# Kernel tuning notes

Measured on AMD Instinct MI355X. Metric: run time of the kernel, lower is better.

Reference implementation:

```python
import jax, jax.numpy as jnp
import numpy as np

EPS = 1e-5

def _weight_quant(w):
    # BitNet b1.58: per-tensor ternary quantization with STE.
    scale = 1.0 / jnp.maximum(jnp.mean(jnp.abs(w)), EPS)
    wq = jnp.clip(jnp.round(w * scale), -1.0, 1.0) / scale
    return w + jax.lax.stop_gradient(wq - w)

def _act_quant(x):
    # per-token int8 absmax quantization with STE.
    scale = 127.0 / jnp.maximum(jnp.max(jnp.abs(x), axis=-1, keepdims=True), EPS)
    xq = jnp.clip(jnp.round(x * scale), -128.0, 127.0) / scale
    return x + jax.lax.stop_gradient(xq - x)

def _bitlinear(x, w):
    # x: [..., in], w: [out, in] (torch layout)
    return jnp.einsum('bsd,hd->bsh', _act_quant(x), _weight_quant(w))

def setup_inputs() -> dict:
    key = jax.random.key(0)
    k1, k2, k3, k4 = jax.random.split(key, 4)
    B, S, D, H = 4, 2048, 2048, 5632
    x = jax.random.normal(k1, (B, S, D), dtype=jnp.float32)
    w1 = jax.random.normal(k2, (H, D), dtype=jnp.float32) * 0.02
    w2 = jax.random.normal(k3, (H, D), dtype=jnp.float32) * 0.02
    w3 = jax.random.normal(k4, (D, H), dtype=jnp.float32) * 0.02
    return {"x": x, "w1": w1, "w2": w2, "w3": w3}

def reference(x, w1, w2, w3):
    gate = jax.nn.silu(_bitlinear(x, w1))   # [B,S,H]
    up = _bitlinear(x, w2)                  # [B,S,H]
    h = gate * up                           # [B,S,H]
    return _bitlinear(h, w3)                # [B,S,D]
```

## Files before the change

### kernel.cpp

```cpp
#include <hip/hip_runtime.h>
#include <hip/hip_bf16.h>
#include <math.h>

#define EPSQ 1e-5f

typedef __attribute__((ext_vector_type(4))) int i32x4;

__device__ __forceinline__ void gload_lds16(const void* g, void* l) {
  __builtin_amdgcn_global_load_lds(
      (__attribute__((address_space(1))) void*)g,
      (__attribute__((address_space(3))) void*)l, 16, 0, 0);
}

__device__ __forceinline__ int clampi8(float v, float lo, float hi) {
  return (int)rintf(fminf(hi, fmaxf(lo, v)));
}

__global__ void wabs3_kernel(const float* __restrict__ w1, const float* __restrict__ w2,
                             const float* __restrict__ w3, int n4,
                             double* __restrict__ sums) {
  const float* w = (blockIdx.y == 0) ? w1 : (blockIdx.y == 1) ? w2 : w3;
  __shared__ double sm[256];
  const float4* w4 = (const float4*)w;
  double acc = 0.0;
  const int stride = gridDim.x * blockDim.x;
  for (int i = blockIdx.x * blockDim.x + threadIdx.x; i < n4; i += stride) {
    float4 v = w4[i];
    acc += (double)fabsf(v.x) + (double)fabsf(v.y) + (double)fabsf(v.z) + (double)fabsf(v.w);
  }
  sm[threadIdx.x] = acc;
  __syncthreads();
  for (int s = 128; s > 0; s >>= 1) {
    if ((int)threadIdx.x < s) sm[threadIdx.x] += sm[threadIdx.x + s];
    __syncthreads();
  }
  if (threadIdx.x == 0) atomicAdd(sums + blockIdx.y, sm[0]);
}

__global__ void wquant3_kernel(const float* __restrict__ w1, const float* __restrict__ w2,
                               const float* __restrict__ w3, int n4,
                               const double* __restrict__ sums, double inv_n,
                               unsigned int* __restrict__ q1, unsigned int* __restrict__ q2,
                               unsigned int* __restrict__ q3) {
  const int wsel = blockIdx.y;
  const float* w = (wsel == 0) ? w1 : (wsel == 1) ? w2 : w3;
  unsigned int* wq = (wsel == 0) ? q1 : (wsel == 1) ? q2 : q3;
  const float s = (float)fmax(sums[wsel] * inv_n, (double)EPSQ);
  const float scale = 1.0f / s;
  const int i = blockIdx.x * blockDim.x + threadIdx.x;
  if (i >= n4) return;
  float4 v = ((const float4*)w)[i];
  const int b0 = clampi8(rintf(v.x * scale), -1.f, 1.f);
  const int b1 = clampi8(rintf(v.y * scale), -1.f, 1.f);
  const int b2 = clampi8(rintf(v.z * scale), -1.f, 1.f);
  const int b3 = clampi8(rintf(v.w * scale), -1.f, 1.f);
  wq[i] = (unsigned int)((b0 & 0xff) | ((b1 & 0xff) << 8) |
                         ((b2 & 0xff) << 16) | ((b3 & 0xff) << 24));
}

__global__ void aquant_kernel(const float* __restrict__ x, int K,
                              unsigned char* __restrict__ q, float* __restrict__ arow) {
  const int row = blockIdx.x;
  const int n4 = K >> 2;
  const float4* xr = (const float4*)(x + (size_t)row * K);
  float m = 0.f;
  for (int c = threadIdx.x; c < n4; c += blockDim.x) {
    float4 v = xr[c];
    m = fmaxf(m, fmaxf(fmaxf(fabsf(v.x), fabsf(v.y)), fmaxf(fabsf(v.z), fabsf(v.w))));
  }
  __shared__ float sm[256];
  sm[threadIdx.x] = m;
  __syncthreads();
  for (int s = 128; s > 0; s >>= 1) {
    if ((int)threadIdx.x < s) sm[threadIdx.x] = fmaxf(sm[threadIdx.x], sm[threadIdx.x + s]);
    __syncthreads();
  }
  const float mv = fmaxf(sm[0], EPSQ);
  const float scale = 127.0f / mv;
  if (threadIdx.x == 0) arow[row] = mv * (1.0f / 127.0f);
  unsigned int* qr = (unsigned int*)(q + (size_t)row * K);
  for (int c = threadIdx.x; c < n4; c += blockDim.x) {
    float4 v = xr[c];
    const int b0 = clampi8(v.x * scale, -128.f, 127.f);
    const int b1 = clampi8(v.y * scale, -128.f, 127.f);
    const int b2 = clampi8(v.z * scale, -128.f, 127.f);
    const int b3 = clampi8(v.w * scale, -128.f, 127.f);
    qr[c] = (unsigned int)((b0 & 0xff) | ((b1 & 0xff) << 8) |
                           ((b2 & 0xff) << 16) | ((b3 & 0xff) << 24));
  }
}

__global__ void aquant_pre_kernel(const float* __restrict__ x, int K,
                                  unsigned char* __restrict__ q, float* __restrict__ arow) {
  const int row = blockIdx.x;
  const float raw = arow[row];
  __syncthreads();
  const float mv = fmaxf(raw, EPSQ);
  const float scale = 127.0f / mv;
  if (threadIdx.x == 0) arow[row] = mv * (1.0f / 127.0f);
  const int n4 = K >> 2;
  const float4* xr = (const float4*)(x + (size_t)row * K);
  unsigned int* qr = (unsigned int*)(q + (size_t)row * K);
  for (int c = threadIdx.x; c < n4; c += blockDim.x) {
    float4 v = xr[c];
    const int b0 = clampi8(v.x * scale, -128.f, 127.f);
    const int b1 = clampi8(v.y * scale, -128.f, 127.f);
    const int b2 = clampi8(v.z * scale, -128.f, 127.f);
    const int b3 = clampi8(v.w * scale, -128.f, 127.f);
    qr[c] = (unsigned int)((b0 & 0xff) | ((b1 & 0xff) << 8) |
                           ((b2 & 0xff) << 16) | ((b3 & 0xff) << 24));
  }
}

#define BKP 64

#define PIPE_BARRIER(N)                                         \
  asm volatile("s_waitcnt vmcnt(" #N ")" ::: "memory");         \
  __builtin_amdgcn_s_barrier();                                 \
  asm volatile("" ::: "memory");

#define GU_SLOT 32768

__launch_bounds__(512, 2)
__global__ void gemm_gateup(const unsigned char* __restrict__ Aq,
                            const unsigned char* __restrict__ W1q,
                            const unsigned char* __restrict__ W2q,
                            const float* __restrict__ arow,
                            const double* __restrict__ wsum,
                            float* __restrict__ Hbuf,
                            float* __restrict__ hmax,
                            const int N, const int K,
                            const int MBb, const int NBb) {
  __shared__ char lds[3 * GU_SLOT];

  const int tid = threadIdx.x;
  const int lane = tid & 63;
  const int wid = tid >> 6;
  const int wm = wid >> 1;
  const int wn = wid & 1;

  const int total = MBb * NBb;
  int swz = blockIdx.x;
  if ((total & 7) == 0) swz = (swz & 7) * (total >> 3) + (swz >> 3);
  const int nb = swz % NBb;
  const int mb = swz / NBb;
  const int m0 = mb * 256;
  const int n0 = nb * 128;

  const unsigned char* Ab  = Aq  + (size_t)m0 * K;
  const unsigned char* B1b = W1q + (size_t)n0 * K;
  const unsigned char* B2b = W2q + (size_t)n0 * K;

  auto stage = [&](int kt, int s) {
    const int k0 = kt * BKP;
    char* base = lds + s * GU_SLOT;
#pragma unroll
    for (int is = 0; is < 2; ++is) {
      const int p = is * 8192 + wid * 1024 + lane * 16;
      const int r = p >> 6;
      const int c = ((p >> 4) & 3) ^ ((r >> 1) & 3);
      gload_lds16(Ab + (size_t)r * K + k0 + c * 16, base + is * 8192 + wid * 1024);
    }
    {
      const int p = wid * 1024 + lane * 16;
      const int r = p >> 6;
      const int c = ((p >> 4) & 3) ^ ((r >> 1) & 3);
      const size_t go = (size_t)r * K + k0 + c * 16;
      gload_lds16(B1b + go, base + 16384 + wid * 1024);
      gload_lds16(B2b + go, base + 24576 + wid * 1024);
    }
  };

  const int c16 = lane >> 4;
  int offA[4], offB1[4], offB2[4];
#pragma unroll
  for (int i = 0; i < 4; ++i) {
    const int row = wm * 64 + i * 16 + (lane & 15);
    offA[i] = row * 64 + ((c16 ^ ((row >> 1) & 3)) << 4);
  }
#pragma unroll
  for (int j = 0; j < 4; ++j) {
    const int n = wn * 64 + j * 16 + (lane & 15);
    const int o = n * 64 + ((c16 ^ ((n >> 1) & 3)) << 4);
    offB1[j] = 16384 + o;
    offB2[j] = 24576 + o;
  }

  i32x4 acc1[4][4] = {};
  i32x4 acc2[4][4] = {};

  const int NT = K / BKP;
  stage(0, 0);
  stage(1, 1);
  PIPE_BARRIER(4)

  int s = 0, s2 = 2;
  for (int t = 0; t < NT; ++t) {
    if (t + 2 < NT) stage(t + 2, s2);
    const char* sb = lds + s * GU_SLOT;
    i32x4 af[4], b1f[4], b2f[4];
#pragma unroll
    for (int i = 0; i < 4; ++i) af[i] = *(const i32x4*)(sb + offA[i]);
#pragma unroll
    for (int j = 0; j < 4; ++j) {
      b1f[j] = *(const i32x4*)(sb + offB1[j]);
      b2f[j] = *(const i32x4*)(sb + offB2[j]);
    }
    __builtin_amdgcn_s_setprio(1);
#pragma unroll
    for (int j = 0; j < 4; ++j)
#pragma unroll
      for (int i = 0; i < 4; ++i) {
        acc1[i][j] = __builtin_amdgcn_mfma_i32_16x16x64_i8(af[i], b1f[j], acc1[i][j], 0, 0, 0);
        acc2[i][j] = __builtin_amdgcn_mfma_i32_16x16x64_i8(af[i], b2f[j], acc2[i][j], 0, 0, 0);
      }
    __builtin_amdgcn_s_setprio(0);
    if (t + 2 < NT) {
      PIPE_BARRIER(4)
    } else if (t + 1 < NT) {
      PIPE_BARRIER(0)
    }
    s = (s == 2) ? 0 : s + 1;
    s2 = (s2 == 2) ? 0 : s2 + 1;
  }

  const double inv_n = 1.0 / 11534336.0;
  const float sw1 = (float)fmax(wsum[0] * inv_n, (double)EPSQ);
  const float sw2 = (float)fmax(wsum[1] * inv_n, (double)EPSQ);
#pragma unroll
  for (int i = 0; i < 4; ++i) {
    const int rb = m0 + wm * 64 + i * 16 + (lane >> 4) * 4;
#pragma unroll
    for (int qe = 0; qe < 4; ++qe) {
      const int grow = rb + qe;
      const float a = arow[grow];
      const float f1 = a * sw1;
      const float f2 = a * sw2;
      float* hr = Hbuf + (size_t)grow * N + n0 + wn * 64 + (lane & 15);
      float lmax = 0.f;
#pragma unroll
      for (int j = 0; j < 4; ++j) {
        const float y1 = (float)acc1[i][j][qe] * f1;
        const float y2 = (float)acc2[i][j][qe] * f2;
        const float h = (y1 / (1.0f + expf(-y1))) * y2;
        hr[j * 16] = h;
        lmax = fmaxf(lmax, fabsf(h));
      }
#pragma unroll
      for (int mk = 8; mk >= 1; mk >>= 1)
        lmax = fmaxf(lmax, __shfl_xor(lmax, mk, 64));
      if ((lane & 15) == 0)
        atomicMax((unsigned int*)(hmax + grow), __float_as_uint(lmax));
    }
  }
}

#define DN_SLOT 24576

__launch_bounds__(512, 2)
__global__ void gemm_down(const unsigned char* __restrict__ Aq,
                          const unsigned char* __restrict__ Wq,
                          const float* __restrict__ arow,
                          const double* __restrict__ wsum,
                          float* __restrict__ Out,
                          const int N, const int K,
                          const int MBb, const int NBb) {
  __shared__ char lds[3 * DN_SLOT];

  const int tid = threadIdx.x;
  const int lane = tid & 63;
  const int wid = tid >> 6;
  const int wm = wid >> 1;
  const int wn = wid & 1;

  const int total = MBb * NBb;
  int swz = blockIdx.x;
  if ((total & 7) == 0) swz = (swz & 7) * (total >> 3) + (swz >> 3);
  const int nb = swz % NBb;
  const int mb = swz / NBb;
  const int m0 = mb * 256;
  const int n0 = nb * 128;

  const unsigned char* Ab = Aq + (size_t)m0 * K;
  const unsigned char* Bb = Wq + (size_t)n0 * K;

  auto stage = [&](int kt, int s) {
    const int k0 = kt * BKP;
    char* base = lds + s * DN_SLOT;
#pragma unroll
    for (int is = 0; is < 2; ++is) {
      const int p = is * 8192 + wid * 1024 + lane * 16;
      const int r = p >> 6;
      const int c = ((p >> 4) & 3) ^ ((r >> 1) & 3);
      gload_lds16(Ab + (size_t)r * K + k0 + c * 16, base + is * 8192 + wid * 1024);
    }
    {
      const int p = wid * 1024 + lane * 16;
      const int r = p >> 6;
      const int c = ((p >> 4) & 3) ^ ((r >> 1) & 3);
      gload_lds16(Bb + (size_t)r * K + k0 + c * 16, base + 16384 + wid * 1024);
    }
  };

  const int c16 = lane >> 4;
  int offA[4], offB[4];
#pragma unroll
  for (int i = 0; i < 4; ++i) {
    const int row = wm * 64 + i * 16 + (lane & 15);
    offA[i] = row * 64 + ((c16 ^ ((row >> 1) & 3)) << 4);
  }
#pragma unroll
  for (int j = 0; j < 4; ++j) {
    const int n = wn * 64 + j * 16 + (lane & 15);
    offB[j] = 16384 + n * 64 + ((c16 ^ ((n >> 1) & 3)) << 4);
  }

  i32x4 acc[4][4] = {};

  const int NT = K / BKP;
  stage(0, 0);
  stage(1, 1);
  PIPE_BARRIER(3)

  int s = 0, s2 = 2;
  for (int t = 0; t < NT; ++t) {
    if (t + 2 < NT) stage(t + 2, s2);
    const char* sb = lds + s * DN_SLOT;
    i32x4 af[4], bf[4];
#pragma unroll
    for (int i = 0; i < 4; ++i) af[i] = *(const i32x4*)(sb + offA[i]);
#pragma unroll
    for (int j = 0; j < 4; ++j) bf[j] = *(const i32x4*)(sb + offB[j]);
    __builtin_amdgcn_s_setprio(1);
#pragma unroll
    for (int j = 0; j < 4; ++j)
#pragma unroll
      for (int i = 0; i < 4; ++i)
        acc[i][j] = __builtin_amdgcn_mfma_i32_16x16x64_i8(af[i], bf[j], acc[i][j], 0, 0, 0);
    __builtin_amdgcn_s_setprio(0);
    if (t + 2 < NT) {
      PIPE_BARRIER(3)
    } else if (t + 1 < NT) {
      PIPE_BARRIER(0)
    }
    s = (s == 2) ? 0 : s + 1;
    s2 = (s2 == 2) ? 0 : s2 + 1;
  }

  const double inv_n = 1.0 / 11534336.0;
  const float sw3 = (float)fmax(wsum[2] * inv_n, (double)EPSQ);
#pragma unroll
  for (int i = 0; i < 4; ++i) {
    const int rb = m0 + wm * 64 + i * 16 + (lane >> 4) * 4;
#pragma unroll
    for (int qe = 0; qe < 4; ++qe) {
      const int grow = rb + qe;
      const float f = arow[grow] * sw3;
      float* orow = Out + (size_t)grow * N + n0 + wn * 64 + (lane & 15);
#pragma unroll
      for (int j = 0; j < 4; ++j) {
        orow[j * 16] = (float)acc[i][j][qe] * f;
      }
    }
  }
}

extern "C" void kernel_launch(void* const* d_in, const int* in_sizes, int n_in,
                              void* d_out, int out_size, void* d_ws, size_t ws_size,
                              hipStream_t stream) {
  (void)n_in; (void)out_size;
  const float* x  = (const float*)d_in[0];
  const float* w1 = (const float*)d_in[1];
  const float* w2 = (const float*)d_in[2];
  const float* w3 = (const float*)d_in[3];
  float* out = (float*)d_out;

  const int D = 2048, H = 5632;
  const int M = in_sizes[0] / D;
  const long long NW = (long long)H * D;

  auto al = [](size_t v) { return (v + 255) & ~(size_t)255; };

  size_t off = 0;
  const size_t o_wsum = off; off += al(3 * sizeof(double));
  const size_t o_w1q  = off; off += al((size_t)NW);
  const size_t o_w2q  = off; off += al((size_t)NW);
  const size_t o_w3q  = off; off += al((size_t)NW);
  const size_t fixed = off;

  int Mc = 256;
  for (int cand = M; cand >= 256; cand >>= 1) {
    size_t need = fixed
                + al((size_t)cand * 4)
                + al((size_t)cand * 4)
                + al((size_t)cand * D)
                + al((size_t)cand * H * 4)
                + al((size_t)cand * H);
    if (need <= ws_size) { Mc = cand; break; }
  }

  size_t coff = fixed;
  const size_t o_arow1 = coff; coff += al((size_t)Mc * 4);
  const size_t o_arow2 = coff; coff += al((size_t)Mc * 4);
  const size_t o_qx    = coff; coff += al((size_t)Mc * D);
  const size_t o_hbuf  = coff; coff += al((size_t)Mc * H * 4);
  const size_t o_qh    = coff; coff += al((size_t)Mc * H);

  char* ws = (char*)d_ws;
  double* wsum        = (double*)(ws + o_wsum);
  unsigned char* w1q  = (unsigned char*)(ws + o_w1q);
  unsigned char* w2q  = (unsigned char*)(ws + o_w2q);
  unsigned char* w3q  = (unsigned char*)(ws + o_w3q);
  float* arow1        = (float*)(ws + o_arow1);
  float* arow2        = (float*)(ws + o_arow2);
  unsigned char* qx   = (unsigned char*)(ws + o_qx);
  float* hbuf         = (float*)(ws + o_hbuf);
  unsigned char* qh   = (unsigned char*)(ws + o_qh);

  hipMemsetAsync(wsum, 0, 3 * sizeof(double), stream);

  const int n4w = (int)(NW / 4);
  wabs3_kernel<<<dim3(1024, 3), 256, 0, stream>>>(w1, w2, w3, n4w, wsum);

  const double inv_n = 1.0 / (double)NW;
  wquant3_kernel<<<dim3(n4w / 256, 3), 256, 0, stream>>>(
      w1, w2, w3, n4w, wsum, inv_n,
      (unsigned int*)w1q, (unsigned int*)w2q, (unsigned int*)w3q);

  const int NBgu = H / 128;
  const int NBdn = D / 128;
  for (int c = 0; c < M; c += Mc) {
    const int MBb = Mc / 256;
    aquant_kernel<<<Mc, 256, 0, stream>>>(x + (size_t)c * D, D, qx, arow1);
    hipMemsetAsync(arow2, 0, (size_t)Mc * 4, stream);
    gemm_gateup<<<MBb * NBgu, 512, 0, stream>>>(qx, w1q, w2q, arow1, wsum,
                                                hbuf, arow2, H, D, MBb, NBgu);
    aquant_pre_kernel<<<Mc, 256, 0, stream>>>(hbuf, H, qh, arow2);
    gemm_down<<<MBb * NBdn, 512, 0, stream>>>(qh, w3q, arow2, wsum,
                                              out + (size_t)c * D, D, H, MBb, NBdn);
  }
}
```

Baseline: 492.8 us.

## Halve GEMM M-tile to 128 and replace atomic row-max with partial-max buffer

Both int8 GEMMs shrink their block tile from 256x128 to 128x128, with 8 waves arranged 2x4 and each wave computing a 64x32 subtile. This cuts LDS per block and doubles the grid, presumably to improve occupancy or load balance. The per-row absmax of the hidden activation is now written as per-slice partials into a new buffer and reduced inside the activation quantization kernel. That replaces the global atomicMax and the memset before it. In exchange, each block gets less operand reuse per loaded byte and the quantization kernel does an extra reduction pass.

```diff
diff --git a/kernel.cpp b/kernel.cpp
--- a/kernel.cpp
+++ b/kernel.cpp
@@ -91,11 +91,20 @@
 }
 
 __global__ void aquant_pre_kernel(const float* __restrict__ x, int K,
+                                  const float* __restrict__ hpart, int nslice,
                                   unsigned char* __restrict__ q, float* __restrict__ arow) {
   const int row = blockIdx.x;
-  const float raw = arow[row];
+  __shared__ float sm[256];
+  float m = 0.f;
+  for (int t = threadIdx.x; t < nslice; t += blockDim.x)
+    m = fmaxf(m, hpart[(size_t)row * nslice + t]);
+  sm[threadIdx.x] = m;
   __syncthreads();
-  const float mv = fmaxf(raw, EPSQ);
+  for (int s = 128; s > 0; s >>= 1) {
+    if ((int)threadIdx.x < s) sm[threadIdx.x] = fmaxf(sm[threadIdx.x], sm[threadIdx.x + s]);
+    __syncthreads();
+  }
+  const float mv = fmaxf(sm[0], EPSQ);
   const float scale = 127.0f / mv;
   if (threadIdx.x == 0) arow[row] = mv * (1.0f / 127.0f);
   const int n4 = K >> 2;
@@ -119,7 +128,7 @@
   __builtin_amdgcn_s_barrier();                                 \
   asm volatile("" ::: "memory");
 
-#define GU_SLOT 32768
+#define GU_SLOT 24576
 
 __launch_bounds__(512, 2)
 __global__ void gemm_gateup(const unsigned char* __restrict__ Aq,
@@ -128,7 +137,7 @@
                             const float* __restrict__ arow,
                             const double* __restrict__ wsum,
                             float* __restrict__ Hbuf,
-                            float* __restrict__ hmax,
+                            float* __restrict__ hpart,
                             const int N, const int K,
                             const int MBb, const int NBb) {
   __shared__ char lds[3 * GU_SLOT];
@@ -136,15 +145,15 @@
   const int tid = threadIdx.x;
   const int lane = tid & 63;
   const int wid = tid >> 6;
-  const int wm = wid >> 1;
-  const int wn = wid & 1;
+  const int wm = wid >> 2;
+  const int wn = wid & 3;
 
   const int total = MBb * NBb;
   int swz = blockIdx.x;
   if ((total & 7) == 0) swz = (swz & 7) * (total >> 3) + (swz >> 3);
   const int nb = swz % NBb;
   const int mb = swz / NBb;
-  const int m0 = mb * 256;
+  const int m0 = mb * 128;
   const int n0 = nb * 128;
 
   const unsigned char* Ab  = Aq  + (size_t)m0 * K;
@@ -154,61 +163,53 @@
   auto stage = [&](int kt, int s) {
     const int k0 = kt * BKP;
     char* base = lds + s * GU_SLOT;
-#pragma unroll
-    for (int is = 0; is < 2; ++is) {
-      const int p = is * 8192 + wid * 1024 + lane * 16;
-      const int r = p >> 6;
-      const int c = ((p >> 4) & 3) ^ ((r >> 1) & 3);
-      gload_lds16(Ab + (size_t)r * K + k0 + c * 16, base + is * 8192 + wid * 1024);
-    }
-    {
-      const int p = wid * 1024 + lane * 16;
-      const int r = p >> 6;
-      const int c = ((p >> 4) & 3) ^ ((r >> 1) & 3);
-      const size_t go = (size_t)r * K + k0 + c * 16;
-      gload_lds16(B1b + go, base + 16384 + wid * 1024);
-      gload_lds16(B2b + go, base + 24576 + wid * 1024);
-    }
+    const int p = wid * 1024 + lane * 16;
+    const int r = p >> 6;
+    const int c = ((p >> 4) & 3) ^ ((r >> 1) & 3);
+    const size_t go = (size_t)r * K + k0 + c * 16;
+    gload_lds16(Ab  + go, base + wid * 1024);
+    gload_lds16(B1b + go, base + 8192 + wid * 1024);
+    gload_lds16(B2b + go, base + 16384 + wid * 1024);
   };
 
   const int c16 = lane >> 4;
-  int offA[4], offB1[4], offB2[4];
+  int offA[4], offB1[2], offB2[2];
 #pragma unroll
   for (int i = 0; i < 4; ++i) {
     const int row = wm * 64 + i * 16 + (lane & 15);
     offA[i] = row * 64 + ((c16 ^ ((row >> 1) & 3)) << 4);
   }
 #pragma unroll
-  for (int j = 0; j < 4; ++j) {
-    const int n = wn * 64 + j * 16 + (lane & 15);
+  for (int j = 0; j < 2; ++j) {
+    const int n = wn * 32 + j * 16 + (lane & 15);
     const int o = n * 64 + ((c16 ^ ((n >> 1) & 3)) << 4);
-    offB1[j] = 16384 + o;
-    offB2[j] = 24576 + o;
-  }
-
-  i32x4 acc1[4][4] = {};
-  i32x4 acc2[4][4] = {};
+    offB1[j] = 8192 + o;
+    offB2[j] = 16384 + o;
+  }
+
+  i32x4 acc1[4][2] = {};
+  i32x4 acc2[4][2] = {};
 
   const int NT = K / BKP;
   stage(0, 0);
   stage(1, 1);
-  PIPE_BARRIER(4)
+  PIPE_BARRIER(3)
 
   int s = 0, s2 = 2;
   for (int t = 0; t < NT; ++t) {
     if (t + 2 < NT) stage(t + 2, s2);
     const char* sb = lds + s * GU_SLOT;
-    i32x4 af[4], b1f[4], b2f[4];
+    i32x4 af[4], b1f[2], b2f[2];
 #pragma unroll
     for (int i = 0; i < 4; ++i) af[i] = *(const i32x4*)(sb + offA[i]);
 #pragma unroll
-    for (int j = 0; j < 4; ++j) {
+    for (int j = 0; j < 2; ++j) {
       b1f[j] = *(const i32x4*)(sb + offB1[j]);
       b2f[j] = *(const i32x4*)(sb + offB2[j]);
     }
     __builtin_amdgcn_s_setprio(1);
 #pragma unroll
-    for (int j = 0; j < 4; ++j)
+    for (int j = 0; j < 2; ++j)
 #pragma unroll
       for (int i = 0; i < 4; ++i) {
         acc1[i][j] = __builtin_amdgcn_mfma_i32_16x16x64_i8(af[i], b1f[j], acc1[i][j], 0, 0, 0);
@@ -216,7 +217,7 @@
       }
     __builtin_amdgcn_s_setprio(0);
     if (t + 2 < NT) {
-      PIPE_BARRIER(4)
+      PIPE_BARRIER(3)
     } else if (t + 1 < NT) {
       PIPE_BARRIER(0)
     }
@@ -227,6 +228,8 @@
   const double inv_n = 1.0 / 11534336.0;
   const float sw1 = (float)fmax(wsum[0] * inv_n, (double)EPSQ);
   const float sw2 = (float)fmax(wsum[1] * inv_n, (double)EPSQ);
+  const int nslice = NBb * 4;
+  const int slice = nb * 4 + wn;
 #pragma unroll
   for (int i = 0; i < 4; ++i) {
     const int rb = m0 + wm * 64 + i * 16 + (lane >> 4) * 4;
@@ -236,10 +239,10 @@
       const float a = arow[grow];
       const float f1 = a * sw1;
       const float f2 = a * sw2;
-      float* hr = Hbuf + (size_t)grow * N + n0 + wn * 64 + (lane & 15);
+      float* hr = Hbuf + (size_t)grow * N + n0 + wn * 32 + (lane & 15);
       float lmax = 0.f;
 #pragma unroll
-      for (int j = 0; j < 4; ++j) {
+      for (int j = 0; j < 2; ++j) {
         const float y1 = (float)acc1[i][j][qe] * f1;
         const float y2 = (float)acc2[i][j][qe] * f2;
         const float h = (y1 / (1.0f + expf(-y1))) * y2;
@@ -250,12 +253,12 @@
       for (int mk = 8; mk >= 1; mk >>= 1)
         lmax = fmaxf(lmax, __shfl_xor(lmax, mk, 64));
       if ((lane & 15) == 0)
-        atomicMax((unsigned int*)(hmax + grow), __float_as_uint(lmax));
+        hpart[(size_t)grow * nslice + slice] = lmax;
     }
   }
 }
 
-#define DN_SLOT 24576
+#define DN_SLOT 16384
 
 __launch_bounds__(512, 2)
 __global__ void gemm_down(const unsigned char* __restrict__ Aq,
@@ -270,15 +273,15 @@
   const int tid = threadIdx.x;
   const int lane = tid & 63;
   const int wid = tid >> 6;
-  const int wm = wid >> 1;
-  const int wn = wid & 1;
+  const int wm = wid >> 2;
+  const int wn = wid & 3;
 
   const int total = MBb * NBb;
   int swz = blockIdx.x;
   if ((total & 7) == 0) swz = (swz & 7) * (total >> 3) + (swz >> 3);
   const int nb = swz % NBb;
   const int mb = swz / NBb;
-  const int m0 = mb * 256;
+  const int m0 = mb * 128;
   const int n0 = nb * 128;
 
   const unsigned char* Ab = Aq + (size_t)m0 * K;
@@ -287,59 +290,52 @@
   auto stage = [&](int kt, int s) {
     const int k0 = kt * BKP;
     char* base = lds + s * DN_SLOT;
-#pragma unroll
-    for (int is = 0; is < 2; ++is) {
-      const int p = is * 8192 + wid * 1024 + lane * 16;
-      const int r = p >> 6;
-      const int c = ((p >> 4) & 3) ^ ((r >> 1) & 3);
-      gload_lds16(Ab + (size_t)r * K + k0 + c * 16, base + is * 8192 + wid * 1024);
-    }
-    {
-      const int p = wid * 1024 + lane * 16;
-      const int r = p >> 6;
-      const int c = ((p >> 4) & 3) ^ ((r >> 1) & 3);
-      gload_lds16(Bb + (size_t)r * K + k0 + c * 16, base + 16384 + wid * 1024);
-    }
+    const int p = wid * 1024 + lane * 16;
+    const int r = p >> 6;
+    const int c = ((p >> 4) & 3) ^ ((r >> 1) & 3);
+    const size_t go = (size_t)r * K + k0 + c * 16;
+    gload_lds16(Ab + go, base + wid * 1024);
+    gload_lds16(Bb + go, base + 8192 + wid * 1024);
   };
 
   const int c16 = lane >> 4;
-  int offA[4], offB[4];
+  int offA[4], offB[2];
 #pragma unroll
   for (int i = 0; i < 4; ++i) {
     const int row = wm * 64 + i * 16 + (lane & 15);
     offA[i] = row * 64 + ((c16 ^ ((row >> 1) & 3)) << 4);
   }
 #pragma unroll
-  for (int j = 0; j < 4; ++j) {
-    const int n = wn * 64 + j * 16 + (lane & 15);
-    offB[j] = 16384 + n * 64 + ((c16 ^ ((n >> 1) & 3)) << 4);
-  }
-
-  i32x4 acc[4][4] = {};
+  for (int j = 0; j < 2; ++j) {
+    const int n = wn * 32 + j * 16 + (lane & 15);
+    offB[j] = 8192 + n * 64 + ((c16 ^ ((n >> 1) & 3)) << 4);
+  }
+
+  i32x4 acc[4][2] = {};
 
   const int NT = K / BKP;
   stage(0, 0);
   stage(1, 1);
-  PIPE_BARRIER(3)
+  PIPE_BARRIER(2)
 
   int s = 0, s2 = 2;
   for (int t = 0; t < NT; ++t) {
     if (t + 2 < NT) stage(t + 2, s2);
     const char* sb = lds + s * DN_SLOT;
-    i32x4 af[4], bf[4];
+    i32x4 af[4], bf[2];
 #pragma unroll
     for (int i = 0; i < 4; ++i) af[i] = *(const i32x4*)(sb + offA[i]);
 #pragma unroll
-    for (int j = 0; j < 4; ++j) bf[j] = *(const i32x4*)(sb + offB[j]);
+    for (int j = 0; j < 2; ++j) bf[j] = *(const i32x4*)(sb + offB[j]);
     __builtin_amdgcn_s_setprio(1);
 #pragma unroll
-    for (int j = 0; j < 4; ++j)
+    for (int j = 0; j < 2; ++j)
 #pragma unroll
       for (int i = 0; i < 4; ++i)
         acc[i][j] = __builtin_amdgcn_mfma_i32_16x16x64_i8(af[i], bf[j], acc[i][j], 0, 0, 0);
     __builtin_amdgcn_s_setprio(0);
     if (t + 2 < NT) {
-      PIPE_BARRIER(3)
+      PIPE_BARRIER(2)
     } else if (t + 1 < NT) {
       PIPE_BARRIER(0)
     }
@@ -356,9 +352,9 @@
     for (int qe = 0; qe < 4; ++qe) {
       const int grow = rb + qe;
       const float f = arow[grow] * sw3;
-      float* orow = Out + (size_t)grow * N + n0 + wn * 64 + (lane & 15);
-#pragma unroll
-      for (int j = 0; j < 4; ++j) {
+      float* orow = Out + (size_t)grow * N + n0 + wn * 32 + (lane & 15);
+#pragma unroll
+      for (int j = 0; j < 2; ++j) {
         orow[j * 16] = (float)acc[i][j][qe] * f;
       }
     }
@@ -378,6 +374,9 @@
   const int D = 2048, H = 5632;
   const int M = in_sizes[0] / D;
   const long long NW = (long long)H * D;
+  const int NBgu = H / 128;
+  const int NBdn = D / 128;
+  const int nslice = NBgu * 4;
 
   auto al = [](size_t v) { return (v + 255) & ~(size_t)255; };
 
@@ -393,6 +392,7 @@
     size_t need = fixed
                 + al((size_t)cand * 4)
                 + al((size_t)cand * 4)
+                + al((size_t)cand * nslice * 4)
                 + al((size_t)cand * D)
                 + al((size_t)cand * H * 4)
                 + al((size_t)cand * H);
@@ -402,6 +402,7 @@
   size_t coff = fixed;
   const size_t o_arow1 = coff; coff += al((size_t)Mc * 4);
   const size_t o_arow2 = coff; coff += al((size_t)Mc * 4);
+  const size_t o_hpart = coff; coff += al((size_t)Mc * nslice * 4);
   const size_t o_qx    = coff; coff += al((size_t)Mc * D);
   const size_t o_hbuf  = coff; coff += al((size_t)Mc * H * 4);
   const size_t o_qh    = coff; coff += al((size_t)Mc * H);
@@ -413,6 +414,7 @@
   unsigned char* w3q  = (unsigned char*)(ws + o_w3q);
   float* arow1        = (float*)(ws + o_arow1);
   float* arow2        = (float*)(ws + o_arow2);
+  float* hpart        = (float*)(ws + o_hpart);
   unsigned char* qx   = (unsigned char*)(ws + o_qx);
   float* hbuf         = (float*)(ws + o_hbuf);
   unsigned char* qh   = (unsigned char*)(ws + o_qh);
@@ -427,15 +429,12 @@
       w1, w2, w3, n4w, wsum, inv_n,
       (unsigned int*)w1q, (unsigned int*)w2q, (unsigned int*)w3q);
 
-  const int NBgu = H / 128;
-  const int NBdn = D / 128;
   for (int c = 0; c < M; c += Mc) {
-    const int MBb = Mc / 256;
+    const int MBb = Mc / 128;
     aquant_kernel<<<Mc, 256, 0, stream>>>(x + (size_t)c * D, D, qx, arow1);
-    hipMemsetAsync(arow2, 0, (size_t)Mc * 4, stream);
     gemm_gateup<<<MBb * NBgu, 512, 0, stream>>>(qx, w1q, w2q, arow1, wsum,
-                                                hbuf, arow2, H, D, MBb, NBgu);
-    aquant_pre_kernel<<<Mc, 256, 0, stream>>>(hbuf, H, qh, arow2);
+                                                hbuf, hpart, H, D, MBb, NBgu);
+    aquant_pre_kernel<<<Mc, 256, 0, stream>>>(hbuf, H, hpart, nslice, qh, arow2);
     gemm_down<<<MBb * NBdn, 512, 0, stream>>>(qh, w3q, arow2, wsum,
                                               out + (size_t)c * D, D, H, MBb, NBdn);
   }
```

New measurement: 528.0 us. +7.1%, slower.
